# Kernel tuning notes

Hardware: AMD Instinct MI355X
Metric: run time of the kernel (lower is better)

Reference implementation:

```python
import math
import jax, jax.numpy as jnp
import numpy as np

B, H, T, D = 1, 4, 1024, 8192  # D = 128 * 256 // 4 (hardcoded module constants)
THETA = 2.0 ** 16


def _frequency(d):
    # quantize(arange(d)) = floor(t/2)*2 ; freq = 1/theta**(q/d)/(2*pi)
    t = jnp.arange(d, dtype=jnp.float32)
    q = jnp.floor(t / 2.0) * 2.0
    return 1.0 / (THETA ** (q / d)) / (2.0 * math.pi)  # [D]


def _rope(v):
    # Faithful to original: slices dim 1 (heads), then row-major reshape back.
    v_rot = jnp.stack([-v[:, 1::2], v[:, ::2]], axis=-1).reshape(v.shape)
    freq = _frequency(v.shape[-1])  # [D]
    phases = jnp.arange(v.shape[2], dtype=jnp.float32)[:, None] * freq[None, :]  # [T, D]
    phases = (phases % 1.0) * (2.0 * math.pi)
    cos = jnp.cos(phases)[None, None]  # [1,1,T,D]
    sin = jnp.sin(phases)[None, None]
    return (v * cos).astype(v.dtype) + (v_rot * sin).astype(v.dtype)


def setup_inputs() -> dict:
    key = jax.random.key(0)
    k1, k2 = jax.random.split(key)
    query = jax.random.normal(k1, (B, H, T, D), dtype=jnp.float32)
    value = jax.random.normal(k2, (B, H, T, D), dtype=jnp.float32)
    return {"query": query, "value": value}


def reference(query, value):
    # key is query (asserted in original)
    q = _rope(query)  # [B,H,T,D]
    scale = 1.0 / math.sqrt(D)
    scores = jnp.einsum('bhtd,bhsd->bhts', q, q) * scale  # [B,H,T,T]
    t_idx = jnp.arange(T)
    causal = t_idx[:, None] > t_idx[None, :]  # tril(diagonal=-1): strictly lower
    scores = jnp.where(causal[None, None], scores, 0.0)
    return jnp.einsum('bhts,bhsd->bhtd', scores, value)
```

## Files before the change

### kernel.cpp

```cpp
#include <hip/hip_runtime.h>
#include <hip/hip_bf16.h>


typedef __bf16 bf16x8 __attribute__((ext_vector_type(8)));
typedef __bf16 bf16x2 __attribute__((ext_vector_type(2)));
typedef float  f32x4  __attribute__((ext_vector_type(4)));

#define HEAD_STRIDE (1024ull * 8192ull)

__device__ inline void gl_lds16(const void* g, void* l) {
  __builtin_amdgcn_global_load_lds(
      (__attribute__((address_space(1))) void*)(g),
      (__attribute__((address_space(3))) void*)(l), 16, 0, 0);
}

__global__ __launch_bounds__(256) void rope_kernel(const float* __restrict__ Q,
                                                   __bf16* __restrict__ Qr) {
  int gid = blockIdx.x * 256 + threadIdx.x;
  size_t e8 = (size_t)gid * 8;
  int d0 = (int)(e8 & 8191);
  int t  = (int)((e8 >> 13) & 1023);
  int h  = (int)(e8 >> 23);

  f32x4 qa = *(const f32x4*)(Q + e8);
  f32x4 qb = *(const f32x4*)(Q + e8 + 4);
  int pt   = t & 1;
  int srct = ((h & 1) << 9) + (t >> 1);
  int sd   = (d0 >> 1) + (pt << 12);
  int hh   = h & ~1;
  size_t soff = ((size_t)srct << 13) + (size_t)sd;
  f32x4 a4 = *(const f32x4*)(Q + (size_t)(hh + 1) * HEAD_STRIDE + soff);
  f32x4 b4 = *(const f32x4*)(Q + (size_t)hh       * HEAD_STRIDE + soff);

  float qv[8];
#pragma unroll
  for (int i = 0; i < 4; ++i) { qv[i] = qa[i]; qv[4 + i] = qb[i]; }

  bf16x8 o;
  float tf = (float)t;
#pragma unroll
  for (int p = 0; p < 4; ++p) {
    float qd = (float)(d0 + 2 * p);
    float fr = exp2f(-qd * (1.0f / 512.0f)) * 0.15915494309189535f;
    float x = tf * fr;
    x -= floorf(x);
    float sn, cs;
    __sincosf(x * 6.283185307179586f, &sn, &cs);
    o[2 * p]     = (__bf16)(qv[2 * p]     * cs - a4[p] * sn);
    o[2 * p + 1] = (__bf16)(qv[2 * p + 1] * cs + b4[p] * sn);
  }
  *(bf16x8*)(Qr + e8) = o;
}

__global__ __launch_bounds__(256) void s1_qqt(const __bf16* __restrict__ Qr,
                                              float* __restrict__ S32) {
  __shared__ __align__(16) __bf16 As[128 * 64];
  __shared__ __align__(16) __bf16 Bs[128 * 64];
  int bid = blockIdx.x;
  int split = bid & 3; bid >>= 2;
  int pair = bid % 36, h = bid / 36;
  int ti = 0, p = pair;
  while (p > ti) { p -= ti + 1; ++ti; }
  int si = p;

  const __bf16* Abase = Qr + (size_t)h * HEAD_STRIDE + ((size_t)(ti * 128) << 13) + split * 2048;
  const __bf16* Bbase = Qr + (size_t)h * HEAD_STRIDE + ((size_t)(si * 128) << 13) + split * 2048;

  int tid = threadIdx.x, lane = tid & 63, wave = tid >> 6;
  int wm = (wave & 1) << 6, wn = (wave >> 1) << 6;
  int l16 = lane & 15, q4 = lane >> 4;
  int srow = lane >> 3, scol = (lane & 7) * 8;

  f32x4 acc[4][4] = {};

  for (int kk = 0; kk < 2048; kk += 64) {
#pragma unroll
    for (int j = 0; j < 4; ++j) {
      int c = wave * 4 + j;
      int row = c * 8 + srow;
      gl_lds16(Abase + (size_t)row * 8192 + kk + scol, &As[c * 512]);
      gl_lds16(Bbase + (size_t)row * 8192 + kk + scol, &Bs[c * 512]);
    }
    __syncthreads();
#pragma unroll
    for (int ks = 0; ks < 64; ks += 32) {
      bf16x8 af[4], bfr[4];
#pragma unroll
      for (int i = 0; i < 4; ++i)
        af[i] = *(const bf16x8*)&As[(wm + i * 16 + l16) * 64 + ks + q4 * 8];
#pragma unroll
      for (int i = 0; i < 4; ++i)
        bfr[i] = *(const bf16x8*)&Bs[(wn + i * 16 + l16) * 64 + ks + q4 * 8];
#pragma unroll
      for (int i = 0; i < 4; ++i)
#pragma unroll
        for (int j = 0; j < 4; ++j)
          acc[i][j] = __builtin_amdgcn_mfma_f32_16x16x32_bf16(af[i], bfr[j], acc[i][j], 0, 0, 0);
    }
    __syncthreads();
  }

  const float scale = 0.011048543456039806f;
  int t_base = ti * 128 + wm, s_base = si * 128 + wn;
  float* Sh = S32 + ((size_t)h << 20);
#pragma unroll
  for (int i = 0; i < 4; ++i)
#pragma unroll
    for (int j = 0; j < 4; ++j) {
      int col = s_base + j * 16 + l16;
#pragma unroll
      for (int r = 0; r < 4; ++r) {
        int row = t_base + i * 16 + q4 * 4 + r;
        if (col < row)
          atomicAdd(&Sh[((size_t)row << 10) + col], acc[i][j][r] * scale);
      }
    }
}

__global__ __launch_bounds__(256) void cvt_kernel(const float* __restrict__ S32,
                                                  __bf16* __restrict__ Sbf) {
  int gid = blockIdx.x * 256 + threadIdx.x;
  size_t e = (size_t)gid * 8;
  f32x4 a = *(const f32x4*)(S32 + e);
  f32x4 b = *(const f32x4*)(S32 + e + 4);
  bf16x8 o;
#pragma unroll
  for (int i = 0; i < 4; ++i) { o[i] = (__bf16)a[i]; o[4 + i] = (__bf16)b[i]; }
  *(bf16x8*)(Sbf + e) = o;
}

__global__ __launch_bounds__(256) void s3_sv(const __bf16* __restrict__ Sbf,
                                             const float* __restrict__ V,
                                             float* __restrict__ out) {
  __shared__ __align__(16) __bf16 As[128 * 64];
  __shared__ __align__(16) __bf16 Bs[128 * 64];
  int bid = blockIdx.x;
  int dt = bid & 63; bid >>= 6;
  int tt = 7 - (bid & 7);
  int h = bid >> 3;

  const __bf16* Abase = Sbf + ((size_t)h << 20) + ((size_t)(tt * 128) << 10);
  const float* Vh = V + (size_t)h * HEAD_STRIDE;
  int dbase = dt * 128;
  int Kmax = tt * 128 + 128;

  int tid = threadIdx.x, lane = tid & 63, wave = tid >> 6;
  int wm = (wave & 1) << 6, wn = (wave >> 1) << 6;
  int l16 = lane & 15, q4 = lane >> 4;
  int srow = lane >> 3, scol = (lane & 7) * 8;
  int q  = tid & 31;
  int pp = tid >> 5;

  f32x4 acc[4][4] = {};

  for (int kk = 0; kk < Kmax; kk += 64) {
#pragma unroll
    for (int j = 0; j < 4; ++j) {
      int c = wave * 4 + j;
      int row = c * 8 + srow;
      gl_lds16(Abase + (size_t)row * 1024 + kk + scol, &As[c * 512]);
    }
#pragma unroll
    for (int pass = 0; pass < 4; ++pass) {
      int s0 = pass * 16 + pp * 2;
      const float* v0p = Vh + (size_t)(kk + s0) * 8192 + dbase;
      const float* v1p = v0p + 8192;
#pragma unroll
      for (int j = 0; j < 4; ++j) {
        int r = q + 32 * j;
        float v0 = v0p[r], v1 = v1p[r];
        int e = r * 64 + (((s0 >> 3) ^ (r & 7)) << 3) + (s0 & 7);
        *(bf16x2*)&Bs[e] = bf16x2{(__bf16)v0, (__bf16)v1};
      }
    }
    __syncthreads();
#pragma unroll
    for (int ks = 0; ks < 64; ks += 32) {
      bf16x8 af[4], bfr[4];
#pragma unroll
      for (int i = 0; i < 4; ++i)
        af[i] = *(const bf16x8*)&As[(wm + i * 16 + l16) * 64 + ks + q4 * 8];
#pragma unroll
      for (int i = 0; i < 4; ++i) {
        int r = wn + i * 16 + l16;
        int oct = ((ks >> 3) + q4) ^ (r & 7);
        bfr[i] = *(const bf16x8*)&Bs[r * 64 + oct * 8];
      }
#pragma unroll
      for (int i = 0; i < 4; ++i)
#pragma unroll
        for (int j = 0; j < 4; ++j)
          acc[i][j] = __builtin_amdgcn_mfma_f32_16x16x32_bf16(af[i], bfr[j], acc[i][j], 0, 0, 0);
    }
    __syncthreads();
  }

  int t_base = tt * 128 + wm, d_base = dbase + wn;
  float* obase = out + (size_t)h * HEAD_STRIDE;
#pragma unroll
  for (int i = 0; i < 4; ++i)
#pragma unroll
    for (int j = 0; j < 4; ++j) {
      int col = d_base + j * 16 + l16;
#pragma unroll
      for (int r = 0; r < 4; ++r) {
        int row = t_base + i * 16 + q4 * 4 + r;
        obase[((size_t)row << 13) + col] = acc[i][j][r];
      }
    }
}

extern "C" void kernel_launch(void* const* d_in, const int* in_sizes, int n_in,
                              void* d_out, int out_size, void* d_ws, size_t ws_size,
                              hipStream_t stream) {
  const float* query = (const float*)d_in[0];
  const float* value = (const float*)d_in[1];
  float* out = (float*)d_out;

  char* ws = (char*)d_ws;
  __bf16* Qr  = (__bf16*)ws;
  float*  S32 = (float*) (ws + 67108864);
  __bf16* Sbf = (__bf16*)(ws + 83886080);

  hipMemsetAsync(S32, 0, 16777216, stream);
  rope_kernel<<<16384, 256, 0, stream>>>(query, Qr);
  s1_qqt<<<576, 256, 0, stream>>>(Qr, S32);
  cvt_kernel<<<2048, 256, 0, stream>>>(S32, Sbf);
  s3_sv<<<2048, 256, 0, stream>>>(Sbf, value, out);
}
```

Baseline: 468.8 us.

## Pre-transpose V to bf16, swizzle LDS tiles, double split-K in QQ^T

A new kernel converts V to bf16 and transposes it into workspace, reusing the Qr buffer once s1 has finished with it. This lets s3_sv stream B tiles with direct global-to-LDS loads in place of strided fp32 scalar loads and per-element conversion. Both GEMMs now use XOR-swizzled LDS layouts to reduce bank conflicts. s1 splits K eight ways instead of four, giving more blocks but twice as many atomics. The cost is an extra pass over V (read 128MB, write 64MB) in exchange for cheaper inner loops.

```diff
diff --git a/kernel.cpp b/kernel.cpp
--- a/kernel.cpp
+++ b/kernel.cpp
@@ -3,7 +3,6 @@
 
 
 typedef __bf16 bf16x8 __attribute__((ext_vector_type(8)));
-typedef __bf16 bf16x2 __attribute__((ext_vector_type(2)));
 typedef float  f32x4  __attribute__((ext_vector_type(4)));
 
 #define HEAD_STRIDE (1024ull * 8192ull)
@@ -57,23 +56,24 @@
   __shared__ __align__(16) __bf16 As[128 * 64];
   __shared__ __align__(16) __bf16 Bs[128 * 64];
   int bid = blockIdx.x;
-  int split = bid & 3; bid >>= 2;
+  int split = bid & 7; bid >>= 3;
   int pair = bid % 36, h = bid / 36;
   int ti = 0, p = pair;
   while (p > ti) { p -= ti + 1; ++ti; }
   int si = p;
 
-  const __bf16* Abase = Qr + (size_t)h * HEAD_STRIDE + ((size_t)(ti * 128) << 13) + split * 2048;
-  const __bf16* Bbase = Qr + (size_t)h * HEAD_STRIDE + ((size_t)(si * 128) << 13) + split * 2048;
+  const __bf16* Abase = Qr + (size_t)h * HEAD_STRIDE + ((size_t)(ti * 128) << 13) + split * 1024;
+  const __bf16* Bbase = Qr + (size_t)h * HEAD_STRIDE + ((size_t)(si * 128) << 13) + split * 1024;
 
   int tid = threadIdx.x, lane = tid & 63, wave = tid >> 6;
   int wm = (wave & 1) << 6, wn = (wave >> 1) << 6;
   int l16 = lane & 15, q4 = lane >> 4;
-  int srow = lane >> 3, scol = (lane & 7) * 8;
+  int srow = lane >> 3;
+  int scol = ((lane & 7) ^ srow) * 8;
 
   f32x4 acc[4][4] = {};
 
-  for (int kk = 0; kk < 2048; kk += 64) {
+  for (int kk = 0; kk < 1024; kk += 64) {
 #pragma unroll
     for (int j = 0; j < 4; ++j) {
       int c = wave * 4 + j;
@@ -86,11 +86,15 @@
     for (int ks = 0; ks < 64; ks += 32) {
       bf16x8 af[4], bfr[4];
 #pragma unroll
-      for (int i = 0; i < 4; ++i)
-        af[i] = *(const bf16x8*)&As[(wm + i * 16 + l16) * 64 + ks + q4 * 8];
-#pragma unroll
-      for (int i = 0; i < 4; ++i)
-        bfr[i] = *(const bf16x8*)&Bs[(wn + i * 16 + l16) * 64 + ks + q4 * 8];
+      for (int i = 0; i < 4; ++i) {
+        int r = wm + i * 16 + l16;
+        af[i] = *(const bf16x8*)&As[r * 64 + (((q4 + (ks >> 3)) ^ (r & 7)) << 3)];
+      }
+#pragma unroll
+      for (int i = 0; i < 4; ++i) {
+        int r = wn + i * 16 + l16;
+        bfr[i] = *(const bf16x8*)&Bs[r * 64 + (((q4 + (ks >> 3)) ^ (r & 7)) << 3)];
+      }
 #pragma unroll
       for (int i = 0; i < 4; ++i)
 #pragma unroll
@@ -129,8 +133,38 @@
   *(bf16x8*)(Sbf + e) = o;
 }
 
+__global__ __launch_bounds__(256) void transp_kernel(const float* __restrict__ V,
+                                                     __bf16* __restrict__ Vt) {
+  __shared__ __bf16 L[64 * 72];
+  int bid = blockIdx.x;
+  int dtile = bid & 127;
+  int st = (bid >> 7) & 15;
+  int h = bid >> 11;
+  int s0 = st << 6, d0 = dtile << 6;
+  const float* Vh = V + (size_t)h * HEAD_STRIDE;
+  __bf16* Vth = Vt + (size_t)h * HEAD_STRIDE;
+  int tid = threadIdx.x;
+  int r = tid >> 2;
+  int c = (tid & 3) << 4;
+#pragma unroll
+  for (int j = 0; j < 4; ++j) {
+    f32x4 v = *(const f32x4*)(Vh + (size_t)(s0 + r) * 8192 + d0 + c + 4 * j);
+#pragma unroll
+    for (int e = 0; e < 4; ++e) L[(c + 4 * j + e) * 72 + r] = (__bf16)v[e];
+  }
+  __syncthreads();
+  int row = tid >> 3;
+  int col8 = (tid & 7) << 3;
+#pragma unroll
+  for (int half = 0; half < 2; ++half) {
+    int dr = row + half * 32;
+    bf16x8 v = *(const bf16x8*)&L[dr * 72 + col8];
+    *(bf16x8*)(Vth + (size_t)(d0 + dr) * 1024 + s0 + col8) = v;
+  }
+}
+
 __global__ __launch_bounds__(256) void s3_sv(const __bf16* __restrict__ Sbf,
-                                             const float* __restrict__ V,
+                                             const __bf16* __restrict__ Vt,
                                              float* __restrict__ out) {
   __shared__ __align__(16) __bf16 As[128 * 64];
   __shared__ __align__(16) __bf16 Bs[128 * 64];
@@ -140,16 +174,14 @@
   int h = bid >> 3;
 
   const __bf16* Abase = Sbf + ((size_t)h << 20) + ((size_t)(tt * 128) << 10);
-  const float* Vh = V + (size_t)h * HEAD_STRIDE;
-  int dbase = dt * 128;
+  const __bf16* Bbase = Vt + (size_t)h * HEAD_STRIDE + ((size_t)(dt * 128) << 10);
   int Kmax = tt * 128 + 128;
 
   int tid = threadIdx.x, lane = tid & 63, wave = tid >> 6;
   int wm = (wave & 1) << 6, wn = (wave >> 1) << 6;
   int l16 = lane & 15, q4 = lane >> 4;
-  int srow = lane >> 3, scol = (lane & 7) * 8;
-  int q  = tid & 31;
-  int pp = tid >> 5;
+  int srow = lane >> 3;
+  int scol = ((lane & 7) ^ srow) * 8;
 
   f32x4 acc[4][4] = {};
 
@@ -159,32 +191,21 @@
       int c = wave * 4 + j;
       int row = c * 8 + srow;
       gl_lds16(Abase + (size_t)row * 1024 + kk + scol, &As[c * 512]);
-    }
-#pragma unroll
-    for (int pass = 0; pass < 4; ++pass) {
-      int s0 = pass * 16 + pp * 2;
-      const float* v0p = Vh + (size_t)(kk + s0) * 8192 + dbase;
-      const float* v1p = v0p + 8192;
-#pragma unroll
-      for (int j = 0; j < 4; ++j) {
-        int r = q + 32 * j;
-        float v0 = v0p[r], v1 = v1p[r];
-        int e = r * 64 + (((s0 >> 3) ^ (r & 7)) << 3) + (s0 & 7);
-        *(bf16x2*)&Bs[e] = bf16x2{(__bf16)v0, (__bf16)v1};
-      }
+      gl_lds16(Bbase + (size_t)row * 1024 + kk + scol, &Bs[c * 512]);
     }
     __syncthreads();
 #pragma unroll
     for (int ks = 0; ks < 64; ks += 32) {
       bf16x8 af[4], bfr[4];
 #pragma unroll
-      for (int i = 0; i < 4; ++i)
-        af[i] = *(const bf16x8*)&As[(wm + i * 16 + l16) * 64 + ks + q4 * 8];
+      for (int i = 0; i < 4; ++i) {
+        int r = wm + i * 16 + l16;
+        af[i] = *(const bf16x8*)&As[r * 64 + (((q4 + (ks >> 3)) ^ (r & 7)) << 3)];
+      }
 #pragma unroll
       for (int i = 0; i < 4; ++i) {
         int r = wn + i * 16 + l16;
-        int oct = ((ks >> 3) + q4) ^ (r & 7);
-        bfr[i] = *(const bf16x8*)&Bs[r * 64 + oct * 8];
+        bfr[i] = *(const bf16x8*)&Bs[r * 64 + (((q4 + (ks >> 3)) ^ (r & 7)) << 3)];
       }
 #pragma unroll
       for (int i = 0; i < 4; ++i)
@@ -195,7 +216,7 @@
     __syncthreads();
   }
 
-  int t_base = tt * 128 + wm, d_base = dbase + wn;
+  int t_base = tt * 128 + wm, d_base = dt * 128 + wn;
   float* obase = out + (size_t)h * HEAD_STRIDE;
 #pragma unroll
   for (int i = 0; i < 4; ++i)
@@ -219,12 +240,14 @@
 
   char* ws = (char*)d_ws;
   __bf16* Qr  = (__bf16*)ws;
+  __bf16* Vt  = (__bf16*)ws;
   float*  S32 = (float*) (ws + 67108864);
   __bf16* Sbf = (__bf16*)(ws + 83886080);
 
   hipMemsetAsync(S32, 0, 16777216, stream);
   rope_kernel<<<16384, 256, 0, stream>>>(query, Qr);
-  s1_qqt<<<576, 256, 0, stream>>>(Qr, S32);
+  s1_qqt<<<1152, 256, 0, stream>>>(Qr, S32);
+  transp_kernel<<<8192, 256, 0, stream>>>(value, Vt);
   cvt_kernel<<<2048, 256, 0, stream>>>(S32, Sbf);
-  s3_sv<<<2048, 256, 0, stream>>>(Sbf, value, out);
-}
+  s3_sv<<<2048, 256, 0, stream>>>(Sbf, Vt, out);
+}
```

Result: no change. 460.2 us (-1.8%).
